# Optimization experiments

Hardware: AMD Instinct MI355X
Metric: run time of the kernel (lower is better)

Reference implementation:

```python
import jax, jax.numpy as jnp
import numpy as np

DIM = 1024
N_HEADS = 16
HEAD_DIM = DIM // N_HEADS
SCALE = HEAD_DIM ** -0.5


def setup_inputs() -> dict:
    key = jax.random.key(0)
    ks = jax.random.split(key, 5)
    x = jax.random.normal(ks[0], (4, 2048, DIM), dtype=jnp.float32)
    s = DIM ** -0.5
    W_qkv = jax.random.normal(ks[1], (DIM, 3 * DIM), dtype=jnp.float32) * s
    b_qkv = jnp.zeros((3 * DIM,), dtype=jnp.float32)
    W_proj = jax.random.normal(ks[2], (DIM, DIM), dtype=jnp.float32) * s
    b_proj = jnp.zeros((DIM,), dtype=jnp.float32)
    return {"x": x, "W_qkv": W_qkv, "b_qkv": b_qkv, "W_proj": W_proj, "b_proj": b_proj}


def reference(x, W_qkv, b_qkv, W_proj, b_proj):
    B, S, D = x.shape
    qkv = x @ W_qkv + b_qkv                      # [B,S,3D]
    qkv = qkv.reshape(B, S, 3, N_HEADS, HEAD_DIM)
    qkv = jnp.transpose(qkv, (2, 0, 3, 1, 4))    # [3,B,H,S,hd]
    q, k, v = qkv[0], qkv[1], qkv[2]
    scores = jnp.einsum('bhqd,bhkd->bhqk', q, k) * SCALE  # [B,H,S,S]
    attn = jax.nn.softmax(scores, axis=-1)
    out = jnp.einsum('bhqk,bhkd->bhqd', attn, v)  # [B,H,S,hd]
    out = jnp.transpose(out, (0, 2, 1, 3)).reshape(B, S, D)
    return out @ W_proj + b_proj
```

## Files before the change

### kernel.cpp

```cpp
#include <hip/hip_runtime.h>

#define DIM   1024
#define SEQ   2048
#define NH    16
#define HD    64

typedef __attribute__((ext_vector_type(8))) short frag_ab;
typedef __attribute__((ext_vector_type(4))) float f32x4;

__device__ __forceinline__ ushort f32_bf16_rne(float f) {
  union { float f; unsigned int u; } v; v.f = f;
  unsigned int u = v.u + 0x7FFFu + ((v.u >> 16) & 1u);
  return (ushort)(u >> 16);
}

__device__ __forceinline__ void split_bf16(float f, ushort& h, ushort& l) {
  h = f32_bf16_rne(f);
  union { unsigned int u; float f; } hv; hv.u = ((unsigned int)h) << 16;
  l = f32_bf16_rne(f - hv.f);
}

__device__ __forceinline__ void gl2lds16(const void* g, void* l) {
  __builtin_amdgcn_global_load_lds(
      (const __attribute__((address_space(1))) unsigned int*)g,
      (__attribute__((address_space(3))) unsigned int*)l, 16, 0, 0);
}

#if __has_builtin(__builtin_amdgcn_exp2f)
#define EXP2F(x) __builtin_amdgcn_exp2f(x)
#else
#define EXP2F(x) exp2f(x)
#endif

__global__ __launch_bounds__(256) void cast_x(const float* __restrict__ x,
                                              ushort* __restrict__ xb) {
  int i = (blockIdx.x * 256 + threadIdx.x) * 8;
  float4 a = *(const float4*)(x + i);
  float4 b = *(const float4*)(x + i + 4);
  uint4 o;
  o.x = (unsigned int)f32_bf16_rne(a.x) | ((unsigned int)f32_bf16_rne(a.y) << 16);
  o.y = (unsigned int)f32_bf16_rne(a.z) | ((unsigned int)f32_bf16_rne(a.w) << 16);
  o.z = (unsigned int)f32_bf16_rne(b.x) | ((unsigned int)f32_bf16_rne(b.y) << 16);
  o.w = (unsigned int)f32_bf16_rne(b.z) | ((unsigned int)f32_bf16_rne(b.w) << 16);
  *(uint4*)(xb + i) = o;
}

template <bool SPLIT>
__global__ __launch_bounds__(256) void tcast(const float* __restrict__ in,
                                             int K, int N,
                                             ushort* __restrict__ outh,
                                             ushort* __restrict__ outl) {
  __shared__ __align__(16) ushort Th[64][72];
  __shared__ __align__(16) ushort Tl[64][72];
  const int kb = blockIdx.y * 64, nb = blockIdx.x * 64;
  const int t = threadIdx.x;
  const int kr = t >> 4, nc = (t & 15) * 4;
#pragma unroll
  for (int j = 0; j < 4; ++j) {
    int k = kr + j * 16;
    float4 v = *(const float4*)&in[(size_t)(kb + k) * N + nb + nc];
    float vv[4] = {v.x, v.y, v.z, v.w};
#pragma unroll
    for (int i = 0; i < 4; ++i) {
      if (SPLIT) {
        ushort h, l; split_bf16(vv[i], h, l);
        Th[nc + i][k] = h; Tl[nc + i][k] = l;
      } else {
        Th[nc + i][k] = f32_bf16_rne(vv[i]);
      }
    }
  }
  __syncthreads();
  const int n = t >> 2, kc = (t & 3) * 16;
  *(uint4*)&outh[(size_t)(nb + n) * K + kb + kc]     = *(const uint4*)&Th[n][kc];
  *(uint4*)&outh[(size_t)(nb + n) * K + kb + kc + 8] = *(const uint4*)&Th[n][kc + 8];
  if (SPLIT) {
    *(uint4*)&outl[(size_t)(nb + n) * K + kb + kc]     = *(const uint4*)&Tl[n][kc];
    *(uint4*)&outl[(size_t)(nb + n) * K + kb + kc + 8] = *(const uint4*)&Tl[n][kc + 8];
  }
}

__global__ __launch_bounds__(256) void qkv_mfma(
    const ushort* __restrict__ Xb, const ushort* __restrict__ Wqt,
    const float* __restrict__ bias,
    ushort* __restrict__ Qw, ushort* __restrict__ Kw, ushort* __restrict__ Vtw) {
  __shared__ __align__(16) ushort As[128 * 32];
  __shared__ __align__(16) ushort Bs[128 * 32];
  const int t = threadIdx.x, wave = t >> 6, lane = t & 63;
  const int ml = lane & 15, quad = lane >> 4;
  const int m0 = blockIdx.y * 128, n0 = blockIdx.x * 128;
  const int wm = (wave & 1) * 64, wn = (wave >> 1) * 64;
  const int srow = lane >> 2, scol = (lane & 3) * 8;
  const int r0 = wave * 16, r1 = (4 + wave) * 16;

  const ushort* Ag = Xb  + (size_t)(m0 + srow) * DIM + scol;
  const ushort* Bg = Wqt + (size_t)(n0 + srow) * DIM + scol;

  f32x4 acc[4][4];
#pragma unroll
  for (int i = 0; i < 4; ++i)
#pragma unroll
    for (int j = 0; j < 4; ++j) acc[i][j] = (f32x4){0.f, 0.f, 0.f, 0.f};

  for (int k0 = 0; k0 < DIM; k0 += 32) {
    __syncthreads();
    gl2lds16(Ag + (size_t)r0 * DIM + k0, &As[r0 * 32]);
    gl2lds16(Ag + (size_t)r1 * DIM + k0, &As[r1 * 32]);
    gl2lds16(Bg + (size_t)r0 * DIM + k0, &Bs[r0 * 32]);
    gl2lds16(Bg + (size_t)r1 * DIM + k0, &Bs[r1 * 32]);
    __syncthreads();
    frag_ab af[4], bfr[4];
#pragma unroll
    for (int im = 0; im < 4; ++im)
      af[im] = *(const frag_ab*)&As[(wm + im * 16 + ml) * 32 + quad * 8];
#pragma unroll
    for (int in_ = 0; in_ < 4; ++in_)
      bfr[in_] = *(const frag_ab*)&Bs[(wn + in_ * 16 + ml) * 32 + quad * 8];
#pragma unroll
    for (int im = 0; im < 4; ++im)
#pragma unroll
      for (int in_ = 0; in_ < 4; ++in_)
        acc[im][in_] = __builtin_amdgcn_mfma_f32_16x16x32_bf16(
            af[im], bfr[in_], acc[im][in_], 0, 0, 0);
  }

  const int t3 = n0 >> 10;
  const int b  = m0 >> 11;
  const int s0 = (m0 & (SEQ - 1)) + wm + quad * 4;
#pragma unroll
  for (int in_ = 0; in_ < 4; ++in_) {
    int n = n0 + wn + in_ * 16 + ml;
    int h = (n >> 6) & 15, d = n & 63;
    float bv = bias[n];
    size_t bh = (size_t)(b * NH + h);
    if (t3 == 2) {
#pragma unroll
      for (int im = 0; im < 4; ++im) {
        int s = s0 + im * 16;
        ushort4 v;
        v.x = f32_bf16_rne(acc[im][in_][0] + bv);
        v.y = f32_bf16_rne(acc[im][in_][1] + bv);
        v.z = f32_bf16_rne(acc[im][in_][2] + bv);
        v.w = f32_bf16_rne(acc[im][in_][3] + bv);
        *(ushort4*)&Vtw[(bh * HD + d) * SEQ + s] = v;
      }
    } else {
      ushort* dst = (t3 == 0) ? Qw : Kw;
#pragma unroll
      for (int im = 0; im < 4; ++im)
#pragma unroll
        for (int r = 0; r < 4; ++r)
          dst[(bh * SEQ + s0 + im * 16 + r) * HD + d] =
              f32_bf16_rne(acc[im][in_][r] + bv);
    }
  }
}

__global__ __launch_bounds__(512, 8) void attn_kernel(
    const ushort* Qw, const ushort* __restrict__ Kw,
    const ushort* __restrict__ Vtw, ushort* Ohw, ushort* Olw) {
  __shared__ __align__(16) ushort KsA[4096], KsB[4096];
  __shared__ __align__(16) ushort VsA[4096], VsB[4096];
  __shared__ __align__(16) ushort PsL[8][1024];

  const int t    = threadIdx.x;
  const int bid  = blockIdx.x;
  const int sbid = (bid & 7) * 128 + (bid >> 3);
  const int bh   = sbid >> 4;
  const int qt   = sbid & 15;
  const int lane = t & 63, wave = t >> 6;
  const int ml   = lane & 15, quad = lane >> 4;
  const int swz  = ml & 7;
  const int lrow = lane >> 3, lw = lane & 7;

  const size_t qbase  = ((size_t)bh * SEQ + qt * 128) * HD;
  const size_t kbase0 = (size_t)bh * SEQ * HD;
  const size_t vbase0 = (size_t)bh * HD * SEQ;

  const frag_ab a_q0 =
      *(const frag_ab*)(Qw + qbase + (size_t)(wave * 16 + ml) * HD + quad * 8);
  const frag_ab a_q1 =
      *(const frag_ab*)(Qw + qbase + (size_t)(wave * 16 + ml) * HD + 32 + quad * 8);

  const ushort* kg = Kw  + kbase0 + (size_t)(wave * 8 + lrow) * HD  + (lw ^ lrow) * 8;
  const ushort* vg = Vtw + vbase0 + (size_t)(wave * 8 + lrow) * SEQ + (lw ^ lrow) * 8;

  gl2lds16(kg, &KsA[wave * 512]);
  gl2lds16(vg, &VsA[wave * 512]);
  __syncthreads();

  f32x4 O[4];
#pragma unroll
  for (int c = 0; c < 4; ++c) O[c] = (f32x4){0.f, 0.f, 0.f, 0.f};
  float lsum = 0.f;
  const float kscale = 0.125f * 1.4426950408889634f;

#define ATTN_STEP(KT, KS_, VS_, KSN, VSN)                                      \
  {                                                                            \
    if ((KT) < 31) {                                                           \
      gl2lds16(kg + (size_t)((KT) + 1) * (64 * HD), &KSN[wave * 512]);         \
      gl2lds16(vg + (size_t)((KT) + 1) * 64,        &VSN[wave * 512]);         \
    }                                                                          \
    f32x4 sc[4];                                                               \
    __builtin_amdgcn_s_setprio(1);                                             \
    _Pragma("unroll")                                                          \
    for (int c = 0; c < 4; ++c) {                                              \
      sc[c] = (f32x4){0.f, 0.f, 0.f, 0.f};                                     \
      frag_ab bk0 = *(const frag_ab*)&KS_[(c * 16 + ml) * 64 +                 \
                                          ((quad ^ swz) * 8)];                 \
      sc[c] = __builtin_amdgcn_mfma_f32_16x16x32_bf16(bk0, a_q0, sc[c], 0, 0, 0); \
      frag_ab bk1 = *(const frag_ab*)&KS_[(c * 16 + ml) * 64 +                 \
                                          (((4 + quad) ^ swz) * 8)];           \
      sc[c] = __builtin_amdgcn_mfma_f32_16x16x32_bf16(bk1, a_q1, sc[c], 0, 0, 0); \
    }                                                                          \
    __builtin_amdgcn_s_setprio(0);                                             \
    _Pragma("unroll")                                                          \
    for (int c = 0; c < 4; ++c) {                                              \
      unsigned int uu[4];                                                      \
      _Pragma("unroll")                                                        \
      for (int r = 0; r < 4; ++r) {                                            \
        float p = EXP2F(fmaf(sc[c][r], kscale, -12.0f));                       \
        union { float f; unsigned int u; } pv_; pv_.f = p;                     \
        unsigned int u = pv_.u & 0xffff0000u;                                  \
        union { unsigned int u; float f; } tf_; tf_.u = u;                     \
        lsum += tf_.f;                                                         \
        uu[r] = u;                                                             \
      }                                                                        \
      unsigned int w0 = (uu[0] >> 16) | (uu[1] & 0xffff0000u);                 \
      unsigned int w1 = (uu[2] >> 16) | (uu[3] & 0xffff0000u);                 \
      int wrd = (c * 2 + (quad >> 1)) ^ swz;                                   \
      char* pdst = (char*)&PsL[wave][0] + ml * 128 + wrd * 16 + (quad & 1) * 8;\
      uint2 wv; wv.x = w0; wv.y = w1;                                          \
      *(uint2*)pdst = wv;                                                      \
    }                                                                          \
    _Pragma("unroll")                                                          \
    for (int ks = 0; ks < 2; ++ks) {                                           \
      frag_ab ap = *(const frag_ab*)((const char*)&PsL[wave][0] + ml * 128 +   \
                                     (((ks * 4 + quad) ^ swz) * 16));          \
      __builtin_amdgcn_s_setprio(1);                                           \
      _Pragma("unroll")                                                        \
      for (int c = 0; c < 4; ++c) {                                            \
        frag_ab bv = *(const frag_ab*)&VS_[(c * 16 + ml) * 64 +                \
                                           (((ks * 4 + quad) ^ swz) * 8)];     \
        O[c] = __builtin_amdgcn_mfma_f32_16x16x32_bf16(ap, bv, O[c], 0, 0, 0); \
      }                                                                        \
      __builtin_amdgcn_s_setprio(0);                                           \
    }                                                                          \
    __syncthreads();                                                           \
  }

  for (int kt = 0; kt < 32; kt += 2) {
    ATTN_STEP(kt,     KsA, VsA, KsB, VsB)
    ATTN_STEP(kt + 1, KsB, VsB, KsA, VsA)
  }
#undef ATTN_STEP

  lsum += __shfl_xor(lsum, 16, 64);
  lsum += __shfl_xor(lsum, 32, 64);
  float linv[4];
#pragma unroll
  for (int r = 0; r < 4; ++r)
    linv[r] = 1.0f / __shfl(lsum, quad * 4 + r, 64);

  const int q0 = qt * 128 + wave * 16 + quad * 4;
#pragma unroll
  for (int r = 0; r < 4; ++r) {
    size_t rowbase = ((size_t)bh * SEQ + q0 + r) * HD;
#pragma unroll
    for (int c = 0; c < 4; ++c) {
      float f = O[c][r] * linv[r];
      ushort h, l; split_bf16(f, h, l);
      Ohw[rowbase + c * 16 + ml] = h;
      Olw[rowbase + c * 16 + ml] = l;
    }
  }
}

__global__ __launch_bounds__(256) void proj_mfma(
    const ushort* __restrict__ Oh, const ushort* __restrict__ Ol,
    const ushort* __restrict__ Wph, const ushort* __restrict__ Wpl,
    const float* __restrict__ bias, float* __restrict__ out) {
  __shared__ __align__(16) ushort As[128 * 32];
  __shared__ __align__(16) ushort Bs[128 * 32];
  const int t = threadIdx.x, wave = t >> 6, lane = t & 63;
  const int ml = lane & 15, quad = lane >> 4;
  const int m0 = blockIdx.y * 128, n0 = blockIdx.x * 128;
  const int wm = (wave & 1) * 64, wn = (wave >> 1) * 64;
  const int srow = lane >> 2, scol = (lane & 3) * 8;
  const int r0 = wave * 16, r1 = (4 + wave) * 16;
  const int b = m0 >> 11, s0r = m0 & (SEQ - 1);

  f32x4 acc[4][4];
#pragma unroll
  for (int i = 0; i < 4; ++i)
#pragma unroll
    for (int j = 0; j < 4; ++j) acc[i][j] = (f32x4){0.f, 0.f, 0.f, 0.f};

  for (int kt = 0; kt < 96; ++kt) {
    int ph = kt >> 5;
    int kv = (kt & 31) * 32;
    const ushort* Asrc = (ph == 1) ? Ol : Oh;
    const ushort* Bsrc = (ph == 2) ? Wpl : Wph;
    int h = kv >> 6, dbase = kv & 63;
    const ushort* Ag = Asrc + (((size_t)(b * NH + h) * SEQ) + s0r + srow) * HD
                            + dbase + scol;
    const ushort* Bg = Bsrc + (size_t)(n0 + srow) * DIM + kv + scol;
    __syncthreads();
    gl2lds16(Ag + (size_t)r0 * HD, &As[r0 * 32]);
    gl2lds16(Ag + (size_t)r1 * HD, &As[r1 * 32]);
    gl2lds16(Bg + (size_t)r0 * DIM, &Bs[r0 * 32]);
    gl2lds16(Bg + (size_t)r1 * DIM, &Bs[r1 * 32]);
    __syncthreads();
    frag_ab af[4], bfr[4];
#pragma unroll
    for (int im = 0; im < 4; ++im)
      af[im] = *(const frag_ab*)&As[(wm + im * 16 + ml) * 32 + quad * 8];
#pragma unroll
    for (int in_ = 0; in_ < 4; ++in_)
      bfr[in_] = *(const frag_ab*)&Bs[(wn + in_ * 16 + ml) * 32 + quad * 8];
#pragma unroll
    for (int im = 0; im < 4; ++im)
#pragma unroll
      for (int in_ = 0; in_ < 4; ++in_)
        acc[im][in_] = __builtin_amdgcn_mfma_f32_16x16x32_bf16(
            af[im], bfr[in_], acc[im][in_], 0, 0, 0);
  }

#pragma unroll
  for (int in_ = 0; in_ < 4; ++in_) {
    int n = n0 + wn + in_ * 16 + ml;
    float bv = bias[n];
#pragma unroll
    for (int im = 0; im < 4; ++im)
#pragma unroll
      for (int r = 0; r < 4; ++r) {
        int m = m0 + wm + im * 16 + quad * 4 + r;
        out[(size_t)m * DIM + n] = acc[im][in_][r] + bv;
      }
  }
}

extern "C" void kernel_launch(void* const* d_in, const int* in_sizes, int n_in,
                              void* d_out, int out_size, void* d_ws, size_t ws_size,
                              hipStream_t stream) {
  const float* x      = (const float*)d_in[0];
  const float* W_qkv  = (const float*)d_in[1];
  const float* b_qkv  = (const float*)d_in[2];
  const float* W_proj = (const float*)d_in[3];
  const float* b_proj = (const float*)d_in[4];
  float* out = (float*)d_out;

  char* ws = (char*)d_ws;
  ushort* Xb  = (ushort*)(ws);
  ushort* Wqt = (ushort*)(ws + 16777216ull);
  ushort* Qw  = (ushort*)(ws + 23068672ull);
  ushort* Kw  = (ushort*)(ws + 39845888ull);
  ushort* Vtw = (ushort*)(ws + 56623104ull);
  ushort* Wph = (ushort*)(ws + 73400320ull);
  ushort* Wpl = (ushort*)(ws + 75497472ull);
  ushort* Ohw = Xb;
  ushort* Olw = Qw;

  cast_x<<<dim3(4096), 256, 0, stream>>>(x, Xb);
  tcast<false><<<dim3(48, 16), 256, 0, stream>>>(W_qkv, DIM, 3 * DIM, Wqt, nullptr);
  tcast<true><<<dim3(16, 16), 256, 0, stream>>>(W_proj, DIM, DIM, Wph, Wpl);
  qkv_mfma<<<dim3(24, 64), 256, 0, stream>>>(Xb, Wqt, b_qkv, Qw, Kw, Vtw);
  attn_kernel<<<dim3(1024), 512, 0, stream>>>(Qw, Kw, Vtw, Ohw, Olw);
  proj_mfma<<<dim3(8, 64), 256, 0, stream>>>(Ohw, Olw, Wph, Wpl, b_proj, out);
}
```

Measured before the change: 336.7 us.

## Widen GEMM K-tile to 64 with XOR-swizzled LDS and grouped block order

In both the QKV and output-projection GEMMs, the K step per LDS stage grows from 32 to 64, which halves the number of barrier pairs per tile. LDS rows are stored with an XOR swizzle on 16-byte chunks to avoid bank conflicts on fragment reads. Block indices are also remapped so that neighbouring workgroups share the same weight column tile, which should improve L2 reuse. The cost is double the LDS footprint, and the index remapping assumes fixed grid dimensions (24x64 and 8x64).

```diff
diff --git a/kernel.cpp b/kernel.cpp
--- a/kernel.cpp
+++ b/kernel.cpp
@@ -84,17 +84,19 @@
     const ushort* __restrict__ Xb, const ushort* __restrict__ Wqt,
     const float* __restrict__ bias,
     ushort* __restrict__ Qw, ushort* __restrict__ Kw, ushort* __restrict__ Vtw) {
-  __shared__ __align__(16) ushort As[128 * 32];
-  __shared__ __align__(16) ushort Bs[128 * 32];
+  __shared__ __align__(16) ushort As[128 * 64];
+  __shared__ __align__(16) ushort Bs[128 * 64];
   const int t = threadIdx.x, wave = t >> 6, lane = t & 63;
   const int ml = lane & 15, quad = lane >> 4;
-  const int m0 = blockIdx.y * 128, n0 = blockIdx.x * 128;
+  const int swz = ml & 7;
+  const int lr = lane >> 3, lc = lane & 7;
+  const int lin = blockIdx.x + blockIdx.y * 24;
+  const int sl  = (lin & 7) * 192 + (lin >> 3);
+  const int m0 = (sl / 24) * 128, n0 = (sl % 24) * 128;
   const int wm = (wave & 1) * 64, wn = (wave >> 1) * 64;
-  const int srow = lane >> 2, scol = (lane & 3) * 8;
-  const int r0 = wave * 16, r1 = (4 + wave) * 16;
-
-  const ushort* Ag = Xb  + (size_t)(m0 + srow) * DIM + scol;
-  const ushort* Bg = Wqt + (size_t)(n0 + srow) * DIM + scol;
+
+  const ushort* Ag = Xb  + (size_t)(m0 + wave * 8 + lr) * DIM + (lc ^ lr) * 8;
+  const ushort* Bg = Wqt + (size_t)(n0 + wave * 8 + lr) * DIM + (lc ^ lr) * 8;
 
   f32x4 acc[4][4];
 #pragma unroll
@@ -102,26 +104,32 @@
 #pragma unroll
     for (int j = 0; j < 4; ++j) acc[i][j] = (f32x4){0.f, 0.f, 0.f, 0.f};
 
-  for (int k0 = 0; k0 < DIM; k0 += 32) {
+  for (int k0 = 0; k0 < DIM; k0 += 64) {
     __syncthreads();
-    gl2lds16(Ag + (size_t)r0 * DIM + k0, &As[r0 * 32]);
-    gl2lds16(Ag + (size_t)r1 * DIM + k0, &As[r1 * 32]);
-    gl2lds16(Bg + (size_t)r0 * DIM + k0, &Bs[r0 * 32]);
-    gl2lds16(Bg + (size_t)r1 * DIM + k0, &Bs[r1 * 32]);
+#pragma unroll
+    for (int i = 0; i < 4; ++i) {
+      gl2lds16(Ag + (size_t)(i * 32) * DIM + k0, &As[(wave * 8 + i * 32) * 64]);
+      gl2lds16(Bg + (size_t)(i * 32) * DIM + k0, &Bs[(wave * 8 + i * 32) * 64]);
+    }
     __syncthreads();
-    frag_ab af[4], bfr[4];
-#pragma unroll
-    for (int im = 0; im < 4; ++im)
-      af[im] = *(const frag_ab*)&As[(wm + im * 16 + ml) * 32 + quad * 8];
-#pragma unroll
-    for (int in_ = 0; in_ < 4; ++in_)
-      bfr[in_] = *(const frag_ab*)&Bs[(wn + in_ * 16 + ml) * 32 + quad * 8];
-#pragma unroll
-    for (int im = 0; im < 4; ++im)
+#pragma unroll
+    for (int kk = 0; kk < 2; ++kk) {
+      frag_ab af[4], bfr[4];
+#pragma unroll
+      for (int im = 0; im < 4; ++im)
+        af[im] = *(const frag_ab*)&As[(wm + im * 16 + ml) * 64 +
+                                      (((kk * 4 + quad) ^ swz) * 8)];
 #pragma unroll
       for (int in_ = 0; in_ < 4; ++in_)
-        acc[im][in_] = __builtin_amdgcn_mfma_f32_16x16x32_bf16(
-            af[im], bfr[in_], acc[im][in_], 0, 0, 0);
+        bfr[in_] = *(const frag_ab*)&Bs[(wn + in_ * 16 + ml) * 64 +
+                                        (((kk * 4 + quad) ^ swz) * 8)];
+#pragma unroll
+      for (int im = 0; im < 4; ++im)
+#pragma unroll
+        for (int in_ = 0; in_ < 4; ++in_)
+          acc[im][in_] = __builtin_amdgcn_mfma_f32_16x16x32_bf16(
+              af[im], bfr[in_], acc[im][in_], 0, 0, 0);
+    }
   }
 
   const int t3 = n0 >> 10;
@@ -280,14 +288,16 @@
     const ushort* __restrict__ Oh, const ushort* __restrict__ Ol,
     const ushort* __restrict__ Wph, const ushort* __restrict__ Wpl,
     const float* __restrict__ bias, float* __restrict__ out) {
-  __shared__ __align__(16) ushort As[128 * 32];
-  __shared__ __align__(16) ushort Bs[128 * 32];
+  __shared__ __align__(16) ushort As[128 * 64];
+  __shared__ __align__(16) ushort Bs[128 * 64];
   const int t = threadIdx.x, wave = t >> 6, lane = t & 63;
   const int ml = lane & 15, quad = lane >> 4;
-  const int m0 = blockIdx.y * 128, n0 = blockIdx.x * 128;
+  const int swz = ml & 7;
+  const int lr = lane >> 3, lc = lane & 7;
+  const int lin = blockIdx.x + blockIdx.y * 8;
+  const int sl  = (lin & 7) * 64 + (lin >> 3);
+  const int m0 = (sl >> 3) * 128, n0 = (sl & 7) * 128;
   const int wm = (wave & 1) * 64, wn = (wave >> 1) * 64;
-  const int srow = lane >> 2, scol = (lane & 3) * 8;
-  const int r0 = wave * 16, r1 = (4 + wave) * 16;
   const int b = m0 >> 11, s0r = m0 & (SEQ - 1);
 
   f32x4 acc[4][4];
@@ -296,34 +306,40 @@
 #pragma unroll
     for (int j = 0; j < 4; ++j) acc[i][j] = (f32x4){0.f, 0.f, 0.f, 0.f};
 
-  for (int kt = 0; kt < 96; ++kt) {
-    int ph = kt >> 5;
-    int kv = (kt & 31) * 32;
+  for (int kt = 0; kt < 48; ++kt) {
+    int ph = kt >> 4;
+    int h  = kt & 15;
+    int kv = h * 64;
     const ushort* Asrc = (ph == 1) ? Ol : Oh;
     const ushort* Bsrc = (ph == 2) ? Wpl : Wph;
-    int h = kv >> 6, dbase = kv & 63;
-    const ushort* Ag = Asrc + (((size_t)(b * NH + h) * SEQ) + s0r + srow) * HD
-                            + dbase + scol;
-    const ushort* Bg = Bsrc + (size_t)(n0 + srow) * DIM + kv + scol;
+    const ushort* Ag = Asrc + (((size_t)(b * NH + h) * SEQ) + s0r + wave * 8 + lr)
+                              * HD + (lc ^ lr) * 8;
+    const ushort* Bg = Bsrc + (size_t)(n0 + wave * 8 + lr) * DIM + kv + (lc ^ lr) * 8;
     __syncthreads();
-    gl2lds16(Ag + (size_t)r0 * HD, &As[r0 * 32]);
-    gl2lds16(Ag + (size_t)r1 * HD, &As[r1 * 32]);
-    gl2lds16(Bg + (size_t)r0 * DIM, &Bs[r0 * 32]);
-    gl2lds16(Bg + (size_t)r1 * DIM, &Bs[r1 * 32]);
+#pragma unroll
+    for (int i = 0; i < 4; ++i) {
+      gl2lds16(Ag + (size_t)(i * 32) * HD,  &As[(wave * 8 + i * 32) * 64]);
+      gl2lds16(Bg + (size_t)(i * 32) * DIM, &Bs[(wave * 8 + i * 32) * 64]);
+    }
     __syncthreads();
-    frag_ab af[4], bfr[4];
-#pragma unroll
-    for (int im = 0; im < 4; ++im)
-      af[im] = *(const frag_ab*)&As[(wm + im * 16 + ml) * 32 + quad * 8];
-#pragma unroll
-    for (int in_ = 0; in_ < 4; ++in_)
-      bfr[in_] = *(const frag_ab*)&Bs[(wn + in_ * 16 + ml) * 32 + quad * 8];
-#pragma unroll
-    for (int im = 0; im < 4; ++im)
+#pragma unroll
+    for (int kk = 0; kk < 2; ++kk) {
+      frag_ab af[4], bfr[4];
+#pragma unroll
+      for (int im = 0; im < 4; ++im)
+        af[im] = *(const frag_ab*)&As[(wm + im * 16 + ml) * 64 +
+                                      (((kk * 4 + quad) ^ swz) * 8)];
 #pragma unroll
       for (int in_ = 0; in_ < 4; ++in_)
-        acc[im][in_] = __builtin_amdgcn_mfma_f32_16x16x32_bf16(
-            af[im], bfr[in_], acc[im][in_], 0, 0, 0);
+        bfr[in_] = *(const frag_ab*)&Bs[(wn + in_ * 16 + ml) * 64 +
+                                        (((kk * 4 + quad) ^ swz) * 8)];
+#pragma unroll
+      for (int im = 0; im < 4; ++im)
+#pragma unroll
+        for (int in_ = 0; in_ < 4; ++in_)
+          acc[im][in_] = __builtin_amdgcn_mfma_f32_16x16x32_bf16(
+              af[im], bfr[in_], acc[im][in_], 0, 0, 0);
+    }
   }
 
 #pragma unroll
```

New measurement: 309.7 us. -8.0%, faster.
